# Kernel optimization log

Hardware: AMD Instinct MI355X
Metric: run time of the kernel (lower is better)

The kernel has to match this reference:

```python
import jax, jax.numpy as jnp
import numpy as np

N, F, E, G = 50000, 128, 1600000, 64
CH = [16, 32, 64, 128, 256]
K = 3
EPS = 1e-5


def setup_inputs() -> dict:
    key = jax.random.key(0)
    ks = jax.random.split(key, 16)
    inp = {}
    inp["x"] = jax.random.normal(ks[0], (N, F), jnp.float32)
    inp["edge_weight"] = jax.random.uniform(ks[1], (E,), jnp.float32)
    inp["edge_index"] = jax.random.randint(ks[2], (2, E), 0, N)
    inp["batch_index"] = jnp.sort(jax.random.randint(ks[3], (N,), 0, G))
    dims = [F] + CH
    i = 4
    for l in range(5):
        fi, fo = dims[l], dims[l + 1]
        inp[f"W{l+1}"] = jax.random.normal(ks[i], (K, fi, fo), jnp.float32) / np.sqrt(K * fi)
        i += 1
        inp[f"b{l+1}"] = jnp.zeros((fo,), jnp.float32)
        if l < 4:  # no BN after the 5th conv
            inp[f"g{l+1}"] = jnp.ones((fo,), jnp.float32)
            inp[f"be{l+1}"] = jnp.zeros((fo,), jnp.float32)
    inp["Wd"] = jax.random.normal(ks[i], (2 * CH[-1], 4), jnp.float32) / np.sqrt(2 * CH[-1])
    inp["bd"] = jnp.zeros((4,), jnp.float32)
    inp["num_graphs"] = G
    return inp


def _bn(h, g, b):
    m = jnp.mean(h, axis=0)
    v = jnp.mean(jnp.square(h - m), axis=0)  # biased variance (torch training mode)
    return g * (h - m) / jnp.sqrt(v + EPS) + b


def reference(x, edge_weight, W1, b1, g1, be1, W2, b2, g2, be2, W3, b3, g3, be3,
              W4, b4, g4, be4, W5, b5, Wd, bd, edge_index, batch_index, num_graphs):
    n = x.shape[0]
    row, col = edge_index[0], edge_index[1]
    # sym-normalized Laplacian, lambda_max=2 -> scaled L_hat has zero diagonal,
    # off-diagonal = -w * deg^-1/2[row] * deg^-1/2[col]
    deg = jax.ops.segment_sum(edge_weight, row, num_segments=n)
    dinv = jnp.where(deg > 0, jax.lax.rsqrt(jnp.where(deg > 0, deg, 1.0)), 0.0)
    norm = -edge_weight * dinv[row] * dinv[col]

    def prop(z):  # L_hat @ z via sparse gather/scatter over edges
        return jax.ops.segment_sum(norm[:, None] * z[col], row, num_segments=n)

    def cheb(z, W, b):  # T0=z, T1=L z, T2=2 L T1 - T0
        t1 = prop(z)
        out = z @ W[0] + t1 @ W[1]
        t2 = 2.0 * prop(t1) - z
        return out + t2 @ W[2] + b

    h = _bn(jax.nn.softplus(cheb(x, W1, b1)), g1, be1)
    h = _bn(jax.nn.softplus(cheb(h, W2, b2)), g2, be2)
    h = _bn(jax.nn.softplus(cheb(h, W3, b3)), g3, be3)
    h = _bn(jax.nn.softplus(cheb(h, W4, b4)), g4, be4)
    h = cheb(h, W5, b5)

    mx = jax.ops.segment_max(h, batch_index, num_segments=num_graphs)
    mx = jnp.where(jnp.isfinite(mx), mx, 0.0)  # guard empty segments
    cnt = jax.ops.segment_sum(jnp.ones((n,), h.dtype), batch_index, num_segments=num_graphs)
    mean = jax.ops.segment_sum(h, batch_index, num_segments=num_graphs) / jnp.maximum(cnt, 1.0)[:, None]
    pooled = jnp.concatenate([mx, mean], axis=1)  # [G, 512]
    logits = pooled @ Wd + bd
    return jax.nn.log_softmax(logits, axis=-1)
```

## Files before the change

kernel.cpp:

```cpp
#include <hip/hip_runtime.h>
#include <hip/hip_fp16.h>
#include <cmath>

#define NN 50000
#define NE 1600000
#define NG 64
#define CAP 96

typedef __attribute__((ext_vector_type(8))) short short8_t;
typedef __attribute__((ext_vector_type(4))) float floatx4;
typedef __attribute__((ext_vector_type(4))) unsigned short us4;

static __device__ __forceinline__ float softplusf(float x) {
    return fmaxf(x, 0.0f) + log1pf(expf(-fabsf(x)));
}

static __device__ __forceinline__ float bf2f(unsigned short u) {
    return __uint_as_float(((unsigned)u) << 16);
}
static __device__ __forceinline__ unsigned short f2bf(float x) {
    unsigned u = __float_as_uint(x);
    unsigned t = (u >> 16) & 1u;
    return (unsigned short)((u + 0x7FFFu + t) >> 16);
}
static __device__ __forceinline__ float h2f(unsigned u) {
    __half_raw r; r.x = (unsigned short)(u & 0xFFFFu);
    return __half2float(__half(r));
}
static __device__ __forceinline__ unsigned short f2h(float x) {
    __half h = __float2half_rn(x);
    return static_cast<__half_raw>(h).x;
}

static __device__ __forceinline__ void split_bf16(float x, unsigned short& hi, unsigned short& lo) {
    unsigned u = __float_as_uint(x);
    unsigned hb = u & 0xFFFF0000u;
    hi = (unsigned short)(hb >> 16);
    float r = x - __uint_as_float(hb);
    lo = f2bf(r);
}

__global__ void k_slot(const int* __restrict__ row, const int* __restrict__ col,
                       const float* __restrict__ w,
                       int* __restrict__ cnt, unsigned* __restrict__ pslots) {
    int e = blockIdx.x * blockDim.x + threadIdx.x;
    if (e < NE) {
        int r = row[e];
        int k = atomicAdd(&cnt[r], 1);
        k = min(k, CAP - 1);
        pslots[(size_t)r * CAP + k] = ((unsigned)col[e] << 16) | (unsigned)f2h(w[e]);
    }
}

__global__ __launch_bounds__(256) void k_degsum(const int* __restrict__ cnt,
                                                const unsigned* __restrict__ pslots,
                                                float* __restrict__ dinv) {
    int tid = threadIdx.x;
    int lane = tid & 15;
    int node = blockIdx.x * 16 + (tid >> 4);
    if (node >= NN) return;
    int e = cnt[node];
    const unsigned* base = pslots + (size_t)node * CAP;
    float s = 0.0f;
    for (int k = lane; k < e; k += 16) s += h2f(base[k]);
#pragma unroll
    for (int m = 8; m >= 1; m >>= 1) s += __shfl_xor(s, m);
    if (lane == 0) dinv[node] = (s > 0.0f) ? rsqrtf(s) : 0.0f;
}

__global__ __launch_bounds__(256) void k_repack(const int* __restrict__ cnt,
                                                unsigned* __restrict__ pslots,
                                                const float* __restrict__ dinv) {
    int tid = threadIdx.x;
    int lane = tid & 15;
    int node = blockIdx.x * 16 + (tid >> 4);
    if (node >= NN) return;
    int e = cnt[node];
    float dr = dinv[node];
    unsigned* pb = pslots + (size_t)node * CAP;
    for (int k = lane; k < e; k += 16) {
        unsigned s = pb[k];
        float wv = -h2f(s) * dr * dinv[s >> 16];
        pb[k] = (s & 0xFFFF0000u) | (unsigned)f2h(wv);
    }
}

__global__ void k_wcat1(const float* __restrict__ W1, float* __restrict__ wc) {
    int i = blockIdx.x * blockDim.x + threadIdx.x;
    if (i < 128 * 48) {
        int k = i / 48, j = i - k * 48;
        float v;
        if (j < 16)      v = W1[k * 16 + j] - W1[2 * 2048 + k * 16 + j];
        else if (j < 32) v = W1[2048 + k * 16 + (j - 16)];
        else             v = W1[2 * 2048 + k * 16 + (j - 32)];
        wc[i] = v;
    }
}

__global__ void k_wsplit(const float* __restrict__ W, int K, int N,
                         unsigned short* __restrict__ hiT, unsigned short* __restrict__ loT) {
    int idx = blockIdx.x * 256 + threadIdx.x;
    if (idx < K * N) {
        int k = idx / N, n = idx - k * N;
        unsigned short h, l;
        split_bf16(W[idx], h, l);
        hiT[(size_t)n * K + k] = h;
        loT[(size_t)n * K + k] = l;
    }
}

#define ASTR 40

__global__ __launch_bounds__(256, 2) void k_gemm_mfma_f32A(
    const float* __restrict__ A, int lda,
    const unsigned short* __restrict__ BhiT,
    const unsigned short* __restrict__ BloT,
    unsigned short* __restrict__ C, int ldc,
    int M, int K, int Ncol)
{
    __shared__ unsigned short Ah[128 * ASTR];
    __shared__ unsigned short Al[128 * ASTR];
    __shared__ unsigned short Bh[128 * ASTR];
    __shared__ unsigned short Bl[128 * ASTR];

    const int tid = threadIdx.x;
    const int lane = tid & 63;
    const int wave = tid >> 6;
    const int wm = wave >> 1, wn = wave & 1;
    const int quad = lane >> 4, l16 = lane & 15;
    const int bm = blockIdx.y * 128, bn = blockIdx.x * 128;
    const int srow = tid >> 1;
    const int skq  = (tid & 1) * 16;

    floatx4 acc[4][4];
#pragma unroll
    for (int i = 0; i < 4; ++i)
#pragma unroll
        for (int j = 0; j < 4; ++j) acc[i][j] = (floatx4){0.f, 0.f, 0.f, 0.f};

    for (int k0 = 0; k0 < K; k0 += 32) {
        float4 a0 = make_float4(0, 0, 0, 0), a1 = a0, a2 = a0, a3 = a0;
        const int ga = bm + srow;
        if (ga < M) {
            const float* Ap = A + (size_t)ga * lda + k0 + skq;
            a0 = *(const float4*)(Ap + 0);
            a1 = *(const float4*)(Ap + 4);
            a2 = *(const float4*)(Ap + 8);
            a3 = *(const float4*)(Ap + 12);
        }
        uint4 bh0 = make_uint4(0, 0, 0, 0), bh1 = bh0, bl0 = bh0, bl1 = bh0;
        const int gb = bn + srow;
        if (gb < Ncol) {
            const unsigned short* ph = BhiT + (size_t)gb * K + k0 + skq;
            const unsigned short* pl = BloT + (size_t)gb * K + k0 + skq;
            bh0 = *(const uint4*)(ph);
            bh1 = *(const uint4*)(ph + 8);
            bl0 = *(const uint4*)(pl);
            bl1 = *(const uint4*)(pl + 8);
        }
        __attribute__((aligned(16))) unsigned short ah[16], al[16];
        const float av[16] = {a0.x, a0.y, a0.z, a0.w, a1.x, a1.y, a1.z, a1.w,
                              a2.x, a2.y, a2.z, a2.w, a3.x, a3.y, a3.z, a3.w};
#pragma unroll
        for (int i = 0; i < 16; ++i) split_bf16(av[i], ah[i], al[i]);

        __syncthreads();
        *(uint4*)&Ah[srow * ASTR + skq]     = *(const uint4*)&ah[0];
        *(uint4*)&Ah[srow * ASTR + skq + 8] = *(const uint4*)&ah[8];
        *(uint4*)&Al[srow * ASTR + skq]     = *(const uint4*)&al[0];
        *(uint4*)&Al[srow * ASTR + skq + 8] = *(const uint4*)&al[8];
        *(uint4*)&Bh[srow * ASTR + skq]     = bh0;
        *(uint4*)&Bh[srow * ASTR + skq + 8] = bh1;
        *(uint4*)&Bl[srow * ASTR + skq]     = bl0;
        *(uint4*)&Bl[srow * ASTR + skq + 8] = bl1;
        __syncthreads();

        short8_t afh[4], afl[4], bfh[4], bfl[4];
#pragma unroll
        for (int t = 0; t < 4; ++t) {
            const int m = wm * 64 + t * 16 + l16;
            afh[t] = *(const short8_t*)&Ah[m * ASTR + quad * 8];
            afl[t] = *(const short8_t*)&Al[m * ASTR + quad * 8];
            const int n = wn * 64 + t * 16 + l16;
            bfh[t] = *(const short8_t*)&Bh[n * ASTR + quad * 8];
            bfl[t] = *(const short8_t*)&Bl[n * ASTR + quad * 8];
        }
#pragma unroll
        for (int i = 0; i < 4; ++i)
#pragma unroll
            for (int j = 0; j < 4; ++j) {
                acc[i][j] = __builtin_amdgcn_mfma_f32_16x16x32_bf16(afh[i], bfh[j], acc[i][j], 0, 0, 0);
                acc[i][j] = __builtin_amdgcn_mfma_f32_16x16x32_bf16(afh[i], bfl[j], acc[i][j], 0, 0, 0);
                acc[i][j] = __builtin_amdgcn_mfma_f32_16x16x32_bf16(afl[i], bfh[j], acc[i][j], 0, 0, 0);
            }
    }

#pragma unroll
    for (int j = 0; j < 4; ++j) {
        const int col = bn + wn * 64 + j * 16 + l16;
        if (col >= Ncol) continue;
#pragma unroll
        for (int i = 0; i < 4; ++i) {
#pragma unroll
            for (int r = 0; r < 4; ++r) {
                const int row = bm + wm * 64 + i * 16 + quad * 4 + r;
                if (row >= M) continue;
                C[(size_t)row * ldc + col] = f2bf(acc[i][j][r]);
            }
        }
    }
}

__global__ __launch_bounds__(256, 2) void k_gemm_mfma_bf(
    const unsigned short* __restrict__ A, int lda,
    const unsigned short* __restrict__ BhiT,
    const unsigned short* __restrict__ BloT,
    void* __restrict__ Cv, int ldc,
    int M, int K, int Ncol,
    const float* __restrict__ bias, int act, int c_f32)
{
    __shared__ unsigned short Ah[128 * ASTR];
    __shared__ unsigned short Bh[128 * ASTR];
    __shared__ unsigned short Bl[128 * ASTR];

    const int tid = threadIdx.x;
    const int lane = tid & 63;
    const int wave = tid >> 6;
    const int wm = wave >> 1, wn = wave & 1;
    const int quad = lane >> 4, l16 = lane & 15;
    const int bm = blockIdx.y * 128, bn = blockIdx.x * 128;
    const int srow = tid >> 1;
    const int skq  = (tid & 1) * 16;

    floatx4 acc[4][4];
#pragma unroll
    for (int i = 0; i < 4; ++i)
#pragma unroll
        for (int j = 0; j < 4; ++j) acc[i][j] = (floatx4){0.f, 0.f, 0.f, 0.f};

    for (int k0 = 0; k0 < K; k0 += 32) {
        uint4 a0 = make_uint4(0, 0, 0, 0), a1 = a0;
        const int ga = bm + srow;
        if (ga < M) {
            const unsigned short* Ap = A + (size_t)ga * lda + k0 + skq;
            a0 = *(const uint4*)(Ap);
            a1 = *(const uint4*)(Ap + 8);
        }
        uint4 bh0 = make_uint4(0, 0, 0, 0), bh1 = bh0, bl0 = bh0, bl1 = bh0;
        const int gb = bn + srow;
        if (gb < Ncol) {
            const unsigned short* ph = BhiT + (size_t)gb * K + k0 + skq;
            const unsigned short* pl = BloT + (size_t)gb * K + k0 + skq;
            bh0 = *(const uint4*)(ph);
            bh1 = *(const uint4*)(ph + 8);
            bl0 = *(const uint4*)(pl);
            bl1 = *(const uint4*)(pl + 8);
        }
        __syncthreads();
        *(uint4*)&Ah[srow * ASTR + skq]     = a0;
        *(uint4*)&Ah[srow * ASTR + skq + 8] = a1;
        *(uint4*)&Bh[srow * ASTR + skq]     = bh0;
        *(uint4*)&Bh[srow * ASTR + skq + 8] = bh1;
        *(uint4*)&Bl[srow * ASTR + skq]     = bl0;
        *(uint4*)&Bl[srow * ASTR + skq + 8] = bl1;
        __syncthreads();

        short8_t afh[4], bfh[4], bfl[4];
#pragma unroll
        for (int t = 0; t < 4; ++t) {
            const int m = wm * 64 + t * 16 + l16;
            afh[t] = *(const short8_t*)&Ah[m * ASTR + quad * 8];
            const int n = wn * 64 + t * 16 + l16;
            bfh[t] = *(const short8_t*)&Bh[n * ASTR + quad * 8];
            bfl[t] = *(const short8_t*)&Bl[n * ASTR + quad * 8];
        }
#pragma unroll
        for (int i = 0; i < 4; ++i)
#pragma unroll
            for (int j = 0; j < 4; ++j) {
                acc[i][j] = __builtin_amdgcn_mfma_f32_16x16x32_bf16(afh[i], bfh[j], acc[i][j], 0, 0, 0);
                acc[i][j] = __builtin_amdgcn_mfma_f32_16x16x32_bf16(afh[i], bfl[j], acc[i][j], 0, 0, 0);
            }
    }

    float* Cf = (float*)Cv;
    unsigned short* Cb = (unsigned short*)Cv;
#pragma unroll
    for (int j = 0; j < 4; ++j) {
        const int col = bn + wn * 64 + j * 16 + l16;
        if (col >= Ncol) continue;
        const float bv = bias ? bias[col] : 0.0f;
#pragma unroll
        for (int i = 0; i < 4; ++i) {
#pragma unroll
            for (int r = 0; r < 4; ++r) {
                const int row = bm + wm * 64 + i * 16 + quad * 4 + r;
                if (row >= M) continue;
                float v = acc[i][j][r] + bv;
                if (act) v = softplusf(v);
                if (c_f32) Cf[(size_t)row * ldc + col] = v;
                else       Cb[(size_t)row * ldc + col] = f2bf(v);
            }
        }
    }
}

__global__ __launch_bounds__(256) void k_gemm(
    const unsigned short* __restrict__ A, int lda,
    const float* __restrict__ B, int ldb,
    unsigned short* __restrict__ C, int ldc,
    int M, int K, int Ncol,
    const float* __restrict__ bias, int act)
{
    __shared__ float As[16][128];
    __shared__ float Bs[16][128];
    const int tid = threadIdx.x;
    const int tx = tid & 15;
    const int ty = tid >> 4;
    const int bm = blockIdx.y * 128;
    const int bn = blockIdx.x * 128;
    const int arow = tid >> 1;
    const int akq = (tid & 1) * 8;
    const int bkr = tid >> 4;
    const int bcq = (tid & 15) * 8;

    float acc[8][8];
#pragma unroll
    for (int i = 0; i < 8; ++i)
#pragma unroll
        for (int j = 0; j < 8; ++j) acc[i][j] = 0.0f;

    for (int k0 = 0; k0 < K; k0 += 16) {
        uint4 ald = make_uint4(0, 0, 0, 0);
        int gr = bm + arow;
        if (gr < M) ald = *(const uint4*)(A + (size_t)gr * lda + k0 + akq);
        float4 b0 = make_float4(0, 0, 0, 0), b1 = make_float4(0, 0, 0, 0);
        int cb = bn + bcq;
        const float* Bp = B + (k0 + bkr) * ldb;
        if (cb < Ncol)     b0 = *(const float4*)(Bp + cb);
        if (cb + 4 < Ncol) b1 = *(const float4*)(Bp + cb + 4);
        __syncthreads();
        const unsigned short* au = (const unsigned short*)&ald;
#pragma unroll
        for (int i = 0; i < 8; ++i) As[akq + i][arow] = bf2f(au[i]);
        *(float4*)&Bs[bkr][bcq] = b0;
        *(float4*)&Bs[bkr][bcq + 4] = b1;
        __syncthreads();
#pragma unroll
        for (int kk = 0; kk < 16; ++kk) {
            float a[8], b[8];
            float4 t;
            t = *(const float4*)&As[kk][ty * 4];      a[0] = t.x; a[1] = t.y; a[2] = t.z; a[3] = t.w;
            t = *(const float4*)&As[kk][64 + ty * 4]; a[4] = t.x; a[5] = t.y; a[6] = t.z; a[7] = t.w;
            t = *(const float4*)&Bs[kk][tx * 4];      b[0] = t.x; b[1] = t.y; b[2] = t.z; b[3] = t.w;
            t = *(const float4*)&Bs[kk][64 + tx * 4]; b[4] = t.x; b[5] = t.y; b[6] = t.z; b[7] = t.w;
#pragma unroll
            for (int i = 0; i < 8; ++i)
#pragma unroll
                for (int j = 0; j < 8; ++j)
                    acc[i][j] = fmaf(a[i], b[j], acc[i][j]);
        }
    }
#pragma unroll
    for (int i = 0; i < 8; ++i) {
        int r = bm + ((i < 4) ? (ty * 4 + i) : (64 + ty * 4 + i - 4));
        if (r >= M) continue;
#pragma unroll
        for (int j = 0; j < 8; ++j) {
            int cl = bn + ((j < 4) ? (tx * 4 + j) : (64 + tx * 4 + j - 4));
            if (cl >= Ncol) continue;
            float v = acc[i][j];
            if (bias) v += bias[cl];
            if (act) v = softplusf(v);
            C[(size_t)r * ldc + cl] = f2bf(v);
        }
    }
}

__global__ __launch_bounds__(256) void k_prop(
    const int* __restrict__ cnt, const unsigned* __restrict__ pslots,
    const unsigned short* __restrict__ z, int zld, int zoff,
    unsigned short* __restrict__ out, int outld, int ooff,
    int ltw, float alpha,
    const unsigned short* __restrict__ add1, int a1ld, int a1off, float c1,
    const unsigned short* __restrict__ add2, int a2ld, int a2off,
    const float* __restrict__ bias, int act)
{
    const int T = 1 << ltw;
    const int lane = threadIdx.x & (T - 1);
    const int node = blockIdx.x * (256 >> ltw) + (threadIdx.x >> ltw);
    if (node >= NN) return;
    const int f4 = lane * 4;
    const int e = cnt[node];
    const unsigned* base = pslots + (size_t)node * CAP;
    float accA[4] = {0, 0, 0, 0};
    float accB[4] = {0, 0, 0, 0};
    const unsigned short* zp = z + zoff + f4;
    int p = 0;
    for (; p + 8 <= e; p += 8) {
        unsigned s0 = base[p + 0], s1 = base[p + 1], s2 = base[p + 2], s3 = base[p + 3];
        unsigned s4 = base[p + 4], s5 = base[p + 5], s6 = base[p + 6], s7 = base[p + 7];
        const us4 z0 = *(const us4*)(zp + (size_t)(s0 >> 16) * zld);
        const us4 z1 = *(const us4*)(zp + (size_t)(s1 >> 16) * zld);
        const us4 z2 = *(const us4*)(zp + (size_t)(s2 >> 16) * zld);
        const us4 z3 = *(const us4*)(zp + (size_t)(s3 >> 16) * zld);
        const us4 z4 = *(const us4*)(zp + (size_t)(s4 >> 16) * zld);
        const us4 z5 = *(const us4*)(zp + (size_t)(s5 >> 16) * zld);
        const us4 z6 = *(const us4*)(zp + (size_t)(s6 >> 16) * zld);
        const us4 z7 = *(const us4*)(zp + (size_t)(s7 >> 16) * zld);
        float w0 = h2f(s0), w1 = h2f(s1), w2 = h2f(s2), w3 = h2f(s3);
        float w4 = h2f(s4), w5 = h2f(s5), w6 = h2f(s6), w7 = h2f(s7);
#pragma unroll
        for (int i = 0; i < 4; ++i) {
            accA[i] = fmaf(w0, bf2f(z0[i]), accA[i]);
            accB[i] = fmaf(w1, bf2f(z1[i]), accB[i]);
            accA[i] = fmaf(w2, bf2f(z2[i]), accA[i]);
            accB[i] = fmaf(w3, bf2f(z3[i]), accB[i]);
            accA[i] = fmaf(w4, bf2f(z4[i]), accA[i]);
            accB[i] = fmaf(w5, bf2f(z5[i]), accB[i]);
            accA[i] = fmaf(w6, bf2f(z6[i]), accA[i]);
            accB[i] = fmaf(w7, bf2f(z7[i]), accB[i]);
        }
    }
    for (; p + 4 <= e; p += 4) {
        unsigned s0 = base[p + 0], s1 = base[p + 1], s2 = base[p + 2], s3 = base[p + 3];
        const us4 z0 = *(const us4*)(zp + (size_t)(s0 >> 16) * zld);
        const us4 z1 = *(const us4*)(zp + (size_t)(s1 >> 16) * zld);
        const us4 z2 = *(const us4*)(zp + (size_t)(s2 >> 16) * zld);
        const us4 z3 = *(const us4*)(zp + (size_t)(s3 >> 16) * zld);
        float w0 = h2f(s0), w1 = h2f(s1), w2 = h2f(s2), w3 = h2f(s3);
#pragma unroll
        for (int i = 0; i < 4; ++i) {
            accA[i] = fmaf(w0, bf2f(z0[i]), accA[i]);
            accB[i] = fmaf(w1, bf2f(z1[i]), accB[i]);
            accA[i] = fmaf(w2, bf2f(z2[i]), accA[i]);
            accB[i] = fmaf(w3, bf2f(z3[i]), accB[i]);
        }
    }
    for (; p < e; ++p) {
        unsigned s = base[p];
        float wv = h2f(s);
        const us4 zv = *(const us4*)(zp + (size_t)(s >> 16) * zld);
#pragma unroll
        for (int i = 0; i < 4; ++i) accA[i] = fmaf(wv, bf2f(zv[i]), accA[i]);
    }
#pragma unroll
    for (int i = 0; i < 4; ++i) accA[i] = alpha * (accA[i] + accB[i]);
    if (add1) {
        const us4 t = *(const us4*)(add1 + (size_t)node * a1ld + a1off + f4);
#pragma unroll
        for (int i = 0; i < 4; ++i) accA[i] = fmaf(c1, bf2f(t[i]), accA[i]);
    }
    if (add2) {
        const us4 t = *(const us4*)(add2 + (size_t)node * a2ld + a2off + f4);
#pragma unroll
        for (int i = 0; i < 4; ++i) accA[i] += bf2f(t[i]);
    }
    if (bias) {
        const float4 t = *(const float4*)(bias + f4);
        accA[0] += t.x; accA[1] += t.y; accA[2] += t.z; accA[3] += t.w;
    }
    if (act) {
#pragma unroll
        for (int i = 0; i < 4; ++i) accA[i] = softplusf(accA[i]);
    }
    us4 o;
#pragma unroll
    for (int i = 0; i < 4; ++i) o[i] = f2bf(accA[i]);
    *(us4*)(out + (size_t)node * outld + ooff + f4) = o;
}

__global__ __launch_bounds__(256) void k_bnstats(const unsigned short* __restrict__ h, int ld, int lc,
                                                 float* __restrict__ stats) {
    const int C = 1 << lc;
    const int tid = threadIdx.x;
    const int c = tid & (C - 1);
    const int rpb = 256 >> lc;
    int r = blockIdx.x * rpb + (tid >> lc);
    const int stride = gridDim.x * rpb;
    float s = 0.0f, q = 0.0f;
    for (; r < NN; r += stride) {
        float v = bf2f(h[(size_t)r * ld + c]);
        s += v;
        q = fmaf(v, v, q);
    }
    __shared__ float shs[256], shq[256];
    shs[tid] = s; shq[tid] = q;
    __syncthreads();
    for (int o = 128; o >= C; o >>= 1) {
        if (tid < o) { shs[tid] += shs[tid + o]; shq[tid] += shq[tid + o]; }
        __syncthreads();
    }
    if (tid < C) {
        atomicAdd(&stats[c], shs[tid]);
        atomicAdd(&stats[128 + c], shq[tid]);
    }
}

__global__ void k_bnapply(unsigned short* __restrict__ h, int ld, int lc,
                          const float* __restrict__ stats,
                          const float* __restrict__ g, const float* __restrict__ be) {
    int idx = blockIdx.x * 256 + threadIdx.x;
    if (idx >= (NN << lc)) return;
    int c = idx & ((1 << lc) - 1);
    int r = idx >> lc;
    const float invN = 1.0f / (float)NN;
    float m = stats[c] * invN;
    float var = fmaf(stats[128 + c], invN, -m * m);
    var = fmaxf(var, 0.0f);
    float inv = rsqrtf(var + 1e-5f);
    float v = bf2f(h[(size_t)r * ld + c]);
    h[(size_t)r * ld + c] = f2bf(fmaf(g[c] * inv, v - m, be[c]));
}

static __device__ __forceinline__ int lower_bound_dev(const int* __restrict__ b, int val) {
    int lo = 0, hi = NN;
    while (lo < hi) {
        int mid = (lo + hi) >> 1;
        if (b[mid] < val) lo = mid + 1; else hi = mid;
    }
    return lo;
}

__global__ void k_gbounds(const int* __restrict__ batch, int* __restrict__ gb) {
    int g = threadIdx.x;
    if (g <= NG) gb[g] = (g == NG) ? NN : lower_bound_dev(batch, g);
}

__global__ __launch_bounds__(256) void k_pool1(const float* __restrict__ h,
                                               const int* __restrict__ gb,
                                               float* __restrict__ partial) {
    int g = blockIdx.y;
    int j = blockIdx.x;
    int start = gb[g], end = gb[g + 1];
    int len = end - start;
    int chunk = (len + 15) >> 4;
    int s = start + j * chunk;
    int e = min(s + chunk, end);
    int c = threadIdx.x;
    float mx = -INFINITY, sum = 0.0f;
    for (int r = s; r < e; ++r) {
        float v = h[(size_t)r * 256 + c];
        mx = fmaxf(mx, v);
        sum += v;
    }
    size_t base = ((size_t)(g * 16 + j)) * 512;
    partial[base + c] = mx;
    partial[base + 256 + c] = sum;
}

__global__ __launch_bounds__(256) void k_pool2d(const float* __restrict__ partial,
                                                const int* __restrict__ gb,
                                                const float* __restrict__ Wd,
                                                const float* __restrict__ bd,
                                                float* __restrict__ out) {
    __shared__ float pl[512];
    __shared__ float red[4][256];
    int g = blockIdx.x;
    int c = threadIdx.x;
    float mx = -INFINITY, sum = 0.0f;
#pragma unroll
    for (int j = 0; j < 16; ++j) {
        size_t base = ((size_t)(g * 16 + j)) * 512;
        mx = fmaxf(mx, partial[base + c]);
        sum += partial[base + 256 + c];
    }
    int len = gb[g + 1] - gb[g];
    pl[c] = (len > 0) ? mx : 0.0f;
    pl[256 + c] = sum / fmaxf((float)len, 1.0f);
    __syncthreads();
    float p[4] = {0, 0, 0, 0};
    for (int k = c; k < 512; k += 256) {
        float pv = pl[k];
#pragma unroll
        for (int cc = 0; cc < 4; ++cc) p[cc] = fmaf(pv, Wd[k * 4 + cc], p[cc]);
    }
#pragma unroll
    for (int cc = 0; cc < 4; ++cc) red[cc][c] = p[cc];
    __syncthreads();
    for (int o = 128; o >= 1; o >>= 1) {
        if (c < o) {
#pragma unroll
            for (int cc = 0; cc < 4; ++cc) red[cc][c] += red[cc][c + o];
        }
        __syncthreads();
    }
    if (c == 0) {
        float l0 = red[0][0] + bd[0], l1 = red[1][0] + bd[1];
        float l2 = red[2][0] + bd[2], l3 = red[3][0] + bd[3];
        float m = fmaxf(fmaxf(l0, l1), fmaxf(l2, l3));
        float ls = m + logf(expf(l0 - m) + expf(l1 - m) + expf(l2 - m) + expf(l3 - m));
        out[g * 4 + 0] = l0 - ls;
        out[g * 4 + 1] = l1 - ls;
        out[g * 4 + 2] = l2 - ls;
        out[g * 4 + 3] = l3 - ls;
    }
}

extern "C" void kernel_launch(void* const* d_in, const int* in_sizes, int n_in,
                              void* d_out, int out_size, void* d_ws, size_t ws_size,
                              hipStream_t stream)
{
    const float* x    = (const float*)d_in[0];
    const float* ew   = (const float*)d_in[1];
    const int*   row  = (const int*)d_in[2];
    const int*   colp = row + NE;
    const int*   batch = (const int*)d_in[3];
    const float* W1 = (const float*)d_in[4];
    const float* b1 = (const float*)d_in[5];
    const float* g1 = (const float*)d_in[6];
    const float* be1 = (const float*)d_in[7];
    const float* W2 = (const float*)d_in[8];
    const float* b2 = (const float*)d_in[9];
    const float* g2 = (const float*)d_in[10];
    const float* be2 = (const float*)d_in[11];
    const float* W3 = (const float*)d_in[12];
    const float* b3 = (const float*)d_in[13];
    const float* g3 = (const float*)d_in[14];
    const float* be3 = (const float*)d_in[15];
    const float* W4 = (const float*)d_in[16];
    const float* b4 = (const float*)d_in[17];
    const float* g4 = (const float*)d_in[18];
    const float* be4 = (const float*)d_in[19];
    const float* W5 = (const float*)d_in[20];
    const float* b5 = (const float*)d_in[21];
    const float* Wd = (const float*)d_in[22];
    const float* bd = (const float*)d_in[23];
    float* outp = (float*)d_out;
    (void)in_sizes; (void)n_in; (void)out_size; (void)ws_size; (void)ew;

    char* wsb = (char*)d_ws;
    size_t off = 0;
    auto take = [&](size_t bytes) -> void* {
        void* p = wsb + off;
        off = (off + bytes + 255) & ~(size_t)255;
        return p;
    };
    int*   cnt    = (int*)take((size_t)NN * sizeof(int));
    float* dinv   = (float*)take((size_t)NN * sizeof(float));
    int*   gb     = (int*)take((NG + 1) * sizeof(int));
    unsigned* pslots = (unsigned*)take((size_t)NN * CAP * sizeof(unsigned));
    float* statsA = (float*)take(4 * 256 * sizeof(float));
    float* wcat   = (float*)take(6144 * sizeof(float));
    unsigned short* bt1h = (unsigned short*)take(48 * 128 * 2);
    unsigned short* bt1l = (unsigned short*)take(48 * 128 * 2);
    unsigned short* bt3h = (unsigned short*)take(64 * 96 * 2);
    unsigned short* bt3l = (unsigned short*)take(64 * 96 * 2);
    unsigned short* bt4h = (unsigned short*)take(128 * 192 * 2);
    unsigned short* bt4l = (unsigned short*)take(128 * 192 * 2);
    unsigned short* bt5h = (unsigned short*)take(256 * 384 * 2);
    unsigned short* bt5l = (unsigned short*)take(256 * 384 * 2);
    float* partial= (float*)take((size_t)NG * 16 * 512 * sizeof(float));
    unsigned short* P   = (unsigned short*)take((size_t)NN * 48 * 2);
    unsigned short* uv  = (unsigned short*)take((size_t)NN * 32 * 2);
    unsigned short* Hc2 = (unsigned short*)take((size_t)NN * 48 * 2);
    unsigned short* Hc3 = (unsigned short*)take((size_t)NN * 96 * 2);
    unsigned short* Hc4 = (unsigned short*)take((size_t)NN * 192 * 2);
    unsigned short* Hc5 = (unsigned short*)take((size_t)NN * 384 * 2);
    float* h5   = (float*)take((size_t)NN * 256 * sizeof(float));

    float* stats1 = statsA;
    float* stats2 = statsA + 256;
    float* stats3 = statsA + 512;
    float* stats4 = statsA + 768;

    hipMemsetAsync(cnt, 0, NN * sizeof(int), stream);
    hipMemsetAsync(statsA, 0, 4 * 256 * sizeof(float), stream);

    k_slot<<<6250, 256, 0, stream>>>(row, colp, ew, cnt, pslots);
    k_degsum<<<3125, 256, 0, stream>>>(cnt, pslots, dinv);
    k_repack<<<3125, 256, 0, stream>>>(cnt, pslots, dinv);

    k_wcat1<<<24, 256, 0, stream>>>(W1, wcat);
    k_gbounds<<<1, 128, 0, stream>>>(batch, gb);
    k_wsplit<<<24, 256, 0, stream>>>(wcat, 128, 48, bt1h, bt1l);
    k_wsplit<<<24, 256, 0, stream>>>(W3, 96, 64, bt3h, bt3l);
    k_wsplit<<<96, 256, 0, stream>>>(W4, 192, 128, bt4h, bt4l);
    k_wsplit<<<384, 256, 0, stream>>>(W5, 384, 256, bt5h, bt5l);

    k_gemm_mfma_f32A<<<dim3(1, 391), 256, 0, stream>>>(x, 128, bt1h, bt1l, P, 48, NN, 128, 48);
    k_prop<<<1563, 256, 0, stream>>>(cnt, pslots, P, 48, 16, uv, 32, 0, 3, 1.0f,
                                     nullptr, 0, 0, 0.0f, nullptr, 0, 0, nullptr, 0);
    k_prop<<<782, 256, 0, stream>>>(cnt, pslots, uv, 32, 16, Hc2, 48, 0, 2, 2.0f,
                                    P, 48, 0, 1.0f, uv, 32, 0, b1, 1);
    k_bnstats<<<256, 256, 0, stream>>>(Hc2, 48, 4, stats1);
    k_bnapply<<<3125, 256, 0, stream>>>(Hc2, 48, 4, stats1, g1, be1);

    k_prop<<<782, 256, 0, stream>>>(cnt, pslots, Hc2, 48, 0, Hc2, 48, 16, 2, 1.0f,
                                    nullptr, 0, 0, 0.0f, nullptr, 0, 0, nullptr, 0);
    k_prop<<<782, 256, 0, stream>>>(cnt, pslots, Hc2, 48, 16, Hc2, 48, 32, 2, 2.0f,
                                    Hc2, 48, 0, -1.0f, nullptr, 0, 0, nullptr, 0);
    k_gemm<<<dim3(1, 391), 256, 0, stream>>>(Hc2, 48, W2, 32, Hc3, 96, NN, 48, 32, b2, 1);
    k_bnstats<<<256, 256, 0, stream>>>(Hc3, 96, 5, stats2);
    k_bnapply<<<6250, 256, 0, stream>>>(Hc3, 96, 5, stats2, g2, be2);

    k_prop<<<1563, 256, 0, stream>>>(cnt, pslots, Hc3, 96, 0, Hc3, 96, 32, 3, 1.0f,
                                     nullptr, 0, 0, 0.0f, nullptr, 0, 0, nullptr, 0);
    k_prop<<<1563, 256, 0, stream>>>(cnt, pslots, Hc3, 96, 32, Hc3, 96, 64, 3, 2.0f,
                                     Hc3, 96, 0, -1.0f, nullptr, 0, 0, nullptr, 0);
    k_gemm_mfma_bf<<<dim3(1, 391), 256, 0, stream>>>(Hc3, 96, bt3h, bt3l, Hc4, 192, NN, 96, 64, b3, 1, 0);
    k_bnstats<<<256, 256, 0, stream>>>(Hc4, 192, 6, stats3);
    k_bnapply<<<12500, 256, 0, stream>>>(Hc4, 192, 6, stats3, g3, be3);

    k_prop<<<3125, 256, 0, stream>>>(cnt, pslots, Hc4, 192, 0, Hc4, 192, 64, 4, 1.0f,
                                     nullptr, 0, 0, 0.0f, nullptr, 0, 0, nullptr, 0);
    k_prop<<<3125, 256, 0, stream>>>(cnt, pslots, Hc4, 192, 64, Hc4, 192, 128, 4, 2.0f,
                                     Hc4, 192, 0, -1.0f, nullptr, 0, 0, nullptr, 0);
    k_gemm_mfma_bf<<<dim3(1, 391), 256, 0, stream>>>(Hc4, 192, bt4h, bt4l, Hc5, 384, NN, 192, 128, b4, 1, 0);
    k_bnstats<<<256, 256, 0, stream>>>(Hc5, 384, 7, stats4);
    k_bnapply<<<25000, 256, 0, stream>>>(Hc5, 384, 7, stats4, g4, be4);

    k_prop<<<6250, 256, 0, stream>>>(cnt, pslots, Hc5, 384, 0, Hc5, 384, 128, 5, 1.0f,
                                     nullptr, 0, 0, 0.0f, nullptr, 0, 0, nullptr, 0);
    k_prop<<<6250, 256, 0, stream>>>(cnt, pslots, Hc5, 384, 128, Hc5, 384, 256, 5, 2.0f,
                                     Hc5, 384, 0, -1.0f, nullptr, 0, 0, nullptr, 0);
    k_gemm_mfma_bf<<<dim3(2, 391), 256, 0, stream>>>(Hc5, 384, bt5h, bt5l, h5, 256, NN, 384, 256, b5, 0, 1);

    k_pool1<<<dim3(16, 64), 256, 0, stream>>>(h5, gb, partial);
    k_pool2d<<<64, 256, 0, stream>>>(partial, gb, Wd, bd, outp);
}
```

Baseline: 841.1 us.

## Partition edge slotting by row range and vectorize batchnorm apply

```diff
diff --git a/kernel.cpp b/kernel.cpp
--- a/kernel.cpp
+++ b/kernel.cpp
@@ -6,10 +6,13 @@
 #define NE 1600000
 #define NG 64
 #define CAP 96
+#define NPART 8
+#define PROWS 6250
 
 typedef __attribute__((ext_vector_type(8))) short short8_t;
 typedef __attribute__((ext_vector_type(4))) float floatx4;
 typedef __attribute__((ext_vector_type(4))) unsigned short us4;
+typedef __attribute__((ext_vector_type(8))) unsigned short us8;
 
 static __device__ __forceinline__ float softplusf(float x) {
     return fmaxf(x, 0.0f) + log1pf(expf(-fabsf(x)));
@@ -40,15 +43,23 @@
     lo = f2bf(r);
 }
 
-__global__ void k_slot(const int* __restrict__ row, const int* __restrict__ col,
-                       const float* __restrict__ w,
-                       int* __restrict__ cnt, unsigned* __restrict__ pslots) {
-    int e = blockIdx.x * blockDim.x + threadIdx.x;
-    if (e < NE) {
+__global__ __launch_bounds__(256) void k_slot2(const int* __restrict__ row,
+                                               const int* __restrict__ col,
+                                               const float* __restrict__ w,
+                                               int* __restrict__ cnt,
+                                               unsigned* __restrict__ pslots) {
+    const int part = blockIdx.x & (NPART - 1);
+    const int bid = blockIdx.x >> 3;
+    const int nb = gridDim.x >> 3;
+    const int rlo = part * PROWS;
+    const int rhi = rlo + PROWS;
+    for (int e = bid * 256 + threadIdx.x; e < NE; e += nb * 256) {
         int r = row[e];
-        int k = atomicAdd(&cnt[r], 1);
-        k = min(k, CAP - 1);
-        pslots[(size_t)r * CAP + k] = ((unsigned)col[e] << 16) | (unsigned)f2h(w[e]);
+        if (r >= rlo && r < rhi) {
+            int k = atomicAdd(&cnt[r], 1);
+            k = min(k, CAP - 1);
+            pslots[(size_t)r * CAP + k] = ((unsigned)col[e] << 16) | (unsigned)f2h(w[e]);
+        }
     }
 }
 
@@ -501,16 +512,24 @@
                           const float* __restrict__ stats,
                           const float* __restrict__ g, const float* __restrict__ be) {
     int idx = blockIdx.x * 256 + threadIdx.x;
-    if (idx >= (NN << lc)) return;
-    int c = idx & ((1 << lc) - 1);
-    int r = idx >> lc;
+    const int C8 = 1 << (lc - 3);
+    if (idx >= NN * C8) return;
+    int r = idx >> (lc - 3);
+    int c0 = (idx & (C8 - 1)) << 3;
     const float invN = 1.0f / (float)NN;
-    float m = stats[c] * invN;
-    float var = fmaf(stats[128 + c], invN, -m * m);
-    var = fmaxf(var, 0.0f);
-    float inv = rsqrtf(var + 1e-5f);
-    float v = bf2f(h[(size_t)r * ld + c]);
-    h[(size_t)r * ld + c] = f2bf(fmaf(g[c] * inv, v - m, be[c]));
+    unsigned short* hp = h + (size_t)r * ld + c0;
+    us8 v = *(const us8*)hp;
+    us8 o;
+#pragma unroll
+    for (int i = 0; i < 8; ++i) {
+        int c = c0 + i;
+        float m = stats[c] * invN;
+        float var = fmaf(stats[128 + c], invN, -m * m);
+        var = fmaxf(var, 0.0f);
+        float inv = rsqrtf(var + 1e-5f);
+        o[i] = f2bf(fmaf(g[c] * inv, bf2f(v[i]) - m, be[c]));
+    }
+    *(us8*)hp = o;
 }
 
 static __device__ __forceinline__ int lower_bound_dev(const int* __restrict__ b, int val) {
@@ -667,7 +686,7 @@
     hipMemsetAsync(cnt, 0, NN * sizeof(int), stream);
     hipMemsetAsync(statsA, 0, 4 * 256 * sizeof(float), stream);
 
-    k_slot<<<6250, 256, 0, stream>>>(row, colp, ew, cnt, pslots);
+    k_slot2<<<2048, 256, 0, stream>>>(row, colp, ew, cnt, pslots);
     k_degsum<<<3125, 256, 0, stream>>>(cnt, pslots, dinv);
     k_repack<<<3125, 256, 0, stream>>>(cnt, pslots, dinv);
 
@@ -684,7 +703,7 @@
     k_prop<<<782, 256, 0, stream>>>(cnt, pslots, uv, 32, 16, Hc2, 48, 0, 2, 2.0f,
                                     P, 48, 0, 1.0f, uv, 32, 0, b1, 1);
     k_bnstats<<<256, 256, 0, stream>>>(Hc2, 48, 4, stats1);
-    k_bnapply<<<3125, 256, 0, stream>>>(Hc2, 48, 4, stats1, g1, be1);
+    k_bnapply<<<391, 256, 0, stream>>>(Hc2, 48, 4, stats1, g1, be1);
 
     k_prop<<<782, 256, 0, stream>>>(cnt, pslots, Hc2, 48, 0, Hc2, 48, 16, 2, 1.0f,
                                     nullptr, 0, 0, 0.0f, nullptr, 0, 0, nullptr, 0);
@@ -692,7 +711,7 @@
                                     Hc2, 48, 0, -1.0f, nullptr, 0, 0, nullptr, 0);
     k_gemm<<<dim3(1, 391), 256, 0, stream>>>(Hc2, 48, W2, 32, Hc3, 96, NN, 48, 32, b2, 1);
     k_bnstats<<<256, 256, 0, stream>>>(Hc3, 96, 5, stats2);
-    k_bnapply<<<6250, 256, 0, stream>>>(Hc3, 96, 5, stats2, g2, be2);
+    k_bnapply<<<782, 256, 0, stream>>>(Hc3, 96, 5, stats2, g2, be2);
 
     k_prop<<<1563, 256, 0, stream>>>(cnt, pslots, Hc3, 96, 0, Hc3, 96, 32, 3, 1.0f,
                                      nullptr, 0, 0, 0.0f, nullptr, 0, 0, nullptr, 0);
@@ -700,7 +719,7 @@
                                      Hc3, 96, 0, -1.0f, nullptr, 0, 0, nullptr, 0);
     k_gemm_mfma_bf<<<dim3(1, 391), 256, 0, stream>>>(Hc3, 96, bt3h, bt3l, Hc4, 192, NN, 96, 64, b3, 1, 0);
     k_bnstats<<<256, 256, 0, stream>>>(Hc4, 192, 6, stats3);
-    k_bnapply<<<12500, 256, 0, stream>>>(Hc4, 192, 6, stats3, g3, be3);
+    k_bnapply<<<1563, 256, 0, stream>>>(Hc4, 192, 6, stats3, g3, be3);
 
     k_prop<<<3125, 256, 0, stream>>>(cnt, pslots, Hc4, 192, 0, Hc4, 192, 64, 4, 1.0f,
                                      nullptr, 0, 0, 0.0f, nullptr, 0, 0, nullptr, 0);
@@ -708,7 +727,7 @@
                                      Hc4, 192, 0, -1.0f, nullptr, 0, 0, nullptr, 0);
     k_gemm_mfma_bf<<<dim3(1, 391), 256, 0, stream>>>(Hc4, 192, bt4h, bt4l, Hc5, 384, NN, 192, 128, b4, 1, 0);
     k_bnstats<<<256, 256, 0, stream>>>(Hc5, 384, 7, stats4);
-    k_bnapply<<<25000, 256, 0, stream>>>(Hc5, 384, 7, stats4, g4, be4);
+    k_bnapply<<<3125, 256, 0, stream>>>(Hc5, 384, 7, stats4, g4, be4);
 
     k_prop<<<6250, 256, 0, stream>>>(cnt, pslots, Hc5, 384, 0, Hc5, 384, 128, 5, 1.0f,
                                      nullptr, 0, 0, 0.0f, nullptr, 0, 0, nullptr, 0);
```

Result: faster. 803.6 us (-4.5%).
